# Kernel tuning notes

Measured on AMD Instinct MI355X. Metric: run time of the kernel, lower is better.

## Reference

```python
import jax, jax.numpy as jnp
import numpy as np

E, N, F = 50000, 25000, 32

def setup_inputs() -> dict:
    key = jax.random.key(0)
    ks = jax.random.split(key, 8)
    efeat = jax.random.normal(ks[0], (E, F), dtype=jnp.float32) * 0.2
    initial_efeats = jax.random.normal(ks[1], (E, F), dtype=jnp.float32) * 0.2
    # msg_fn / attn_fn: Linear(F, F*F)
    Wm = jax.random.normal(ks[2], (F * F, F), dtype=jnp.float32) * 0.05
    bm = jnp.zeros((F * F,), dtype=jnp.float32)
    Wa = jax.random.normal(ks[3], (F * F, F), dtype=jnp.float32) * 0.05
    ba = jnp.zeros((F * F,), dtype=jnp.float32)
    src = jax.random.randint(ks[4], (E,), 0, N, dtype=jnp.int32)
    dst = jax.random.randint(ks[5], (E,), 0, N, dtype=jnp.int32)
    return {"efeat": efeat, "initial_efeats": initial_efeats, "Wm": Wm, "bm": bm,
            "Wa": Wa, "ba": ba, "src": src, "dst": dst, "num_nodes": N}

def reference(efeat, initial_efeats, Wm, bm, Wa, ba, src, dst, num_nodes):
    e, f = efeat.shape
    # edge-conditioned transform matrices: [E, F, F]
    w_m = (efeat @ Wm.T + bm).reshape(e, f, f)
    w_a = (efeat @ Wa.T + ba).reshape(e, f, f)
    h = efeat[:, :, None]                 # [E, F, 1]
    ih = initial_efeats[:, :, None]       # [E, F, 1]
    e1 = w_m * h                          # [E, F, F]
    exp_e2 = jnp.exp(w_a * h)             # [E, F, F]
    initial_e1 = w_m * ih
    exp_initial_e2 = jnp.exp(w_a * ih)
    # scatter-sum exp weights to destination nodes, gather back at src
    sum_exp_node = jax.ops.segment_sum(exp_e2, dst, num_segments=num_nodes)  # [N, F, F]
    sum_exp = sum_exp_node[src] - exp_e2 + exp_initial_e2
    h1 = exp_e2 * e1
    initial_h1 = exp_initial_e2 * initial_e1
    m_node = jax.ops.segment_sum(h1, dst, num_segments=num_nodes)            # [N, F, F]
    h2 = (m_node[src] - h1 + initial_h1) / sum_exp
    return h2.sum(axis=1)                 # [E, F]
```

## Files before the change

kernel.cpp:

```cpp
#include <hip/hip_runtime.h>
#include <hip/hip_fp16.h>
#include <math.h>
#include <stdint.h>


#define FDIM   32
#define NNODES 25000

typedef __attribute__((ext_vector_type(8))) short bf16x8;
typedef __attribute__((ext_vector_type(4))) float f32x4;

__device__ __forceinline__ unsigned short f2bf(float f) {
    unsigned u = __float_as_uint(f);
    return (unsigned short)((u + 0x7FFFu + ((u >> 16) & 1u)) >> 16);
}
__device__ __forceinline__ float hlo(unsigned v) {
    return __half2float(__ushort_as_half((unsigned short)v));
}
__device__ __forceinline__ unsigned pk2(float m, float a) {
    unsigned um = (unsigned)__half_as_ushort(__float2half(m));
    unsigned ua = (unsigned)__half_as_ushort(__float2half(a));
    return (um >> 8) | (ua & 0xFF00u);
}

__global__ __launch_bounds__(256) void zero_f4(float4* __restrict__ p, int n4) {
    int i = blockIdx.x * blockDim.x + threadIdx.x;
    int stride = gridDim.x * blockDim.x;
    float4 z = make_float4(0.f, 0.f, 0.f, 0.f);
    for (; i < n4; i += stride) p[i] = z;
}

__global__ __launch_bounds__(256) void k_hist(
    const int* __restrict__ src, const int* __restrict__ dst,
    int* __restrict__ cnt_src, int* __restrict__ cnt_dst, int E) {
    int e = blockIdx.x * blockDim.x + threadIdx.x;
    if (e < E) {
        atomicAdd(&cnt_dst[dst[e]], 1);
        atomicAdd(&cnt_src[src[e]], 1);
    }
}

__global__ __launch_bounds__(256) void k_scan2(
    const int* __restrict__ cnt_dst, int* __restrict__ off_dst, int* __restrict__ cur_dst,
    const int* __restrict__ cnt_src, int* __restrict__ off_src, int* __restrict__ cur_src,
    int n) {
    const int* cnt = blockIdx.x ? cnt_src : cnt_dst;
    int* off = blockIdx.x ? off_src : off_dst;
    int* cur = blockIdx.x ? cur_src : cur_dst;
    __shared__ int wsum[4];
    __shared__ int carry_sh;
    const int tid = threadIdx.x, lane = tid & 63, w = tid >> 6;
    if (tid == 0) carry_sh = 0;
    __syncthreads();
    for (int base = 0; base < n; base += 1024) {
        int i0 = base + tid * 4;
        int v0 = (i0 + 0 < n) ? cnt[i0 + 0] : 0;
        int v1 = (i0 + 1 < n) ? cnt[i0 + 1] : 0;
        int v2 = (i0 + 2 < n) ? cnt[i0 + 2] : 0;
        int v3 = (i0 + 3 < n) ? cnt[i0 + 3] : 0;
        int s = v0 + v1 + v2 + v3;
        int inc = s;
        for (int d = 1; d < 64; d <<= 1) {
            int t = __shfl_up(inc, d, 64);
            if (lane >= d) inc += t;
        }
        if (lane == 63) wsum[w] = inc;
        __syncthreads();
        int wbase = 0;
        for (int k = 0; k < w; ++k) wbase += wsum[k];
        int carry = carry_sh;
        int excl = carry + wbase + inc - s;
        if (i0 + 0 < n) { off[i0 + 0] = excl; cur[i0 + 0] = excl; } excl += v0;
        if (i0 + 1 < n) { off[i0 + 1] = excl; cur[i0 + 1] = excl; } excl += v1;
        if (i0 + 2 < n) { off[i0 + 2] = excl; cur[i0 + 2] = excl; } excl += v2;
        if (i0 + 3 < n) { off[i0 + 3] = excl; cur[i0 + 3] = excl; }
        __syncthreads();
        if (tid == 255) carry_sh = carry + wbase + inc;
    }
    __syncthreads();
    if (tid == 0) off[n] = carry_sh;
}

__global__ __launch_bounds__(256) void k_scatter(
    const int* __restrict__ src, const int* __restrict__ dst,
    int* __restrict__ cur_src, int* __restrict__ cur_dst,
    int* __restrict__ eb_src, int* __restrict__ eb_dst, int E) {
    int e = blockIdx.x * blockDim.x + threadIdx.x;
    if (e < E) {
        int p = atomicAdd(&cur_dst[dst[e]], 1); eb_dst[p] = e;
        int q = atomicAdd(&cur_src[src[e]], 1); eb_src[q] = e;
    }
}

__global__ __launch_bounds__(256) void prep_w(
    const float* __restrict__ Wm, const float* __restrict__ Wa,
    short* __restrict__ wbuf) {
    int idx = blockIdx.x * blockDim.x + threadIdx.x;
    if (idx >= 2 * 64 * 64) return;
    int mat  = idx >> 12;
    int jt   = (idx >> 6) & 63;
    int lane = idx & 63;
    const float* W = mat ? Wa : Wm;
    const float* s = W + (size_t)(jt * 16 + (lane & 15)) * FDIM + (lane >> 4) * 8;
    bf16x8 v;
#pragma unroll
    for (int t = 0; t < 8; ++t) v[t] = (short)f2bf(s[t]);
    *(bf16x8*)(wbuf + (size_t)idx * 8) = v;
}

__global__ __launch_bounds__(256) void gemm(
    const float* __restrict__ efeat,
    const float* __restrict__ bm, const float* __restrict__ ba,
    const short* __restrict__ wbuf,
    unsigned short* __restrict__ buf, int E)
{
    const int lane = threadIdx.x & 63;
    const int wid  = threadIdx.x >> 6;
    const int et   = blockIdx.x * 4 + wid;
    if (et * 16 >= E) return;
    const int r16 = lane & 15;
    const int kq  = lane >> 4;

    const float* xa = efeat + (size_t)(et * 16 + r16) * FDIM + kq * 8;
    bf16x8 xfrag;
#pragma unroll
    for (int t = 0; t < 8; ++t) xfrag[t] = (short)f2bf(xa[t]);

    const int e = et * 16 + r16;
    unsigned* bout = (unsigned*)(buf + (size_t)e * 1024);

    for (int jt = 0; jt < 64; ++jt) {
        bf16x8 wfm = *(const bf16x8*)(wbuf + ((size_t)(jt)      * 64 + lane) * 8);
        bf16x8 wfa = *(const bf16x8*)(wbuf + ((size_t)(64 + jt) * 64 + lane) * 8);
        const int jb = jt * 16 + kq * 4;
        const float4 bm4 = *(const float4*)(bm + jb);
        const float4 ba4 = *(const float4*)(ba + jb);
        f32x4 accm = {bm4.x, bm4.y, bm4.z, bm4.w};
        f32x4 acca = {ba4.x, ba4.y, ba4.z, ba4.w};
        accm = __builtin_amdgcn_mfma_f32_16x16x32_bf16(wfm, xfrag, accm, 0, 0, 0);
        acca = __builtin_amdgcn_mfma_f32_16x16x32_bf16(wfa, xfrag, acca, 0, 0, 0);
        unsigned p0 = pk2(accm[0], acca[0]);
        unsigned p1 = pk2(accm[1], acca[1]);
        unsigned p2 = pk2(accm[2], acca[2]);
        unsigned p3 = pk2(accm[3], acca[3]);
        unsigned long long v = (unsigned long long)(p0 | (p1 << 16)) |
                               ((unsigned long long)(p2 | (p3 << 16)) << 32);
        *(unsigned long long*)(bout + (jb >> 1)) = v;
    }
}

__global__ __launch_bounds__(256) void consume(
    const float* __restrict__ efeat, const float* __restrict__ ifeat,
    const unsigned short* __restrict__ buf,
    const int* __restrict__ off_dst, const int* __restrict__ eb_dst,
    const int* __restrict__ off_src, const int* __restrict__ eb_src,
    float* __restrict__ out)
{
    const int tid = threadIdx.x;
    const int l   = tid & 63;
    const int wid = tid >> 6;
    const int n   = blockIdx.x * 4 + wid;
    if (n >= NNODES) return;

    const int a0 = off_dst[n], a1 = off_dst[n + 1];
    const int b0 = off_src[n], b1 = off_src[n + 1];
    const int din = a1 - a0, dout = b1 - b0;
    if (dout == 0) return;

    int eid = (l < 32) ? eb_dst[a0 + l] : eb_src[b0 + (l - 32)];
    const int i = l >> 1;

    float S[16], M[16];
#pragma unroll
    for (int t = 0; t < 16; ++t) { S[t] = 0.f; M[t] = 0.f; }

    for (int t = 0; t < din; ++t) {
        int e = (t < 32) ? __shfl(eid, t, 64) : eb_dst[a0 + t];
        e = __builtin_amdgcn_readfirstlane(e);
        const uint4* bp = (const uint4*)(buf + ((size_t)e << 10) + l * 16);
        uint4 d0 = bp[0], d1 = bp[1];
        float xi = efeat[((size_t)e << 5) + i];
        unsigned u[8] = {d0.x, d0.y, d0.z, d0.w, d1.x, d1.y, d1.z, d1.w};
#pragma unroll
        for (int w = 0; w < 8; ++w) {
            unsigned uu = u[w];
            float am0 = hlo(uu << 8),  aa0 = hlo(uu);
            float am1 = hlo(uu >> 8),  aa1 = hlo(uu >> 16);
            float ea = __expf(aa0 * xi);
            float eb = __expf(aa1 * xi);
            S[2 * w]     += ea;  M[2 * w]     = fmaf(ea, am0 * xi, M[2 * w]);
            S[2 * w + 1] += eb;  M[2 * w + 1] = fmaf(eb, am1 * xi, M[2 * w + 1]);
        }
    }

    for (int t = 0; t < dout; ++t) {
        int e = (t < 32) ? __shfl(eid, 32 + t, 64) : eb_src[b0 + t];
        e = __builtin_amdgcn_readfirstlane(e);
        const uint4* bp = (const uint4*)(buf + ((size_t)e << 10) + l * 16);
        uint4 d0 = bp[0], d1 = bp[1];
        float xi  = efeat[((size_t)e << 5) + i];
        float x0i = ifeat[((size_t)e << 5) + i];
        unsigned u[8] = {d0.x, d0.y, d0.z, d0.w, d1.x, d1.y, d1.z, d1.w};
        float acc[16];
#pragma unroll
        for (int w = 0; w < 8; ++w) {
            unsigned uu = u[w];
            float am0 = hlo(uu << 8),  aa0 = hlo(uu);
            float am1 = hlo(uu >> 8),  aa1 = hlo(uu >> 16);
#define PROC(T2, AM, AA)                                                \
            {                                                           \
                float amx  = (AM) * xi;                                 \
                float e2   = __expf((AA) * xi);                         \
                float h1   = e2 * amx;                                  \
                float ei2  = __expf((AA) * x0i);                        \
                float ih1  = ei2 * ((AM) * x0i);                        \
                float den  = (S[T2] - e2) + ei2;                        \
                float num  = (M[T2] - h1) + ih1;                        \
                float h2   = num * __builtin_amdgcn_rcpf(den);          \
                acc[T2] = isfinite(h2) ? h2 : 0.f;                      \
            }
            PROC(2 * w,     am0, aa0);
            PROC(2 * w + 1, am1, aa1);
#undef PROC
        }
#pragma unroll
        for (int t2 = 0; t2 < 16; ++t2) {
            acc[t2] += __shfl_xor(acc[t2], 2, 64);
            acc[t2] += __shfl_xor(acc[t2], 4, 64);
            acc[t2] += __shfl_xor(acc[t2], 8, 64);
            acc[t2] += __shfl_xor(acc[t2], 16, 64);
            acc[t2] += __shfl_xor(acc[t2], 32, 64);
        }
        if (l < 2) {
            float4* o = (float4*)(out + ((size_t)e << 5) + l * 16);
            o[0] = make_float4(acc[0],  acc[1],  acc[2],  acc[3]);
            o[1] = make_float4(acc[4],  acc[5],  acc[6],  acc[7]);
            o[2] = make_float4(acc[8],  acc[9],  acc[10], acc[11]);
            o[3] = make_float4(acc[12], acc[13], acc[14], acc[15]);
        }
    }
}

extern "C" void kernel_launch(void* const* d_in, const int* in_sizes, int n_in,
                              void* d_out, int out_size, void* d_ws, size_t ws_size,
                              hipStream_t stream) {
    const float* efeat = (const float*)d_in[0];
    const float* ifeat = (const float*)d_in[1];
    const float* Wm    = (const float*)d_in[2];
    const float* bm    = (const float*)d_in[3];
    const float* Wa    = (const float*)d_in[4];
    const float* ba    = (const float*)d_in[5];
    const int*   src   = (const int*)d_in[6];
    const int*   dst   = (const int*)d_in[7];
    const int E = in_sizes[6];
    const int N = NNODES;
    float* out = (float*)d_out;

    int* cnt_dst = (int*)d_ws;
    int* cnt_src = cnt_dst + N;
    int* off_dst = cnt_src + N;
    int* off_src = off_dst + (N + 1);
    int* cur_dst = off_src + (N + 1);
    int* cur_src = cur_dst + N;
    int* eb_dst  = cur_src + N;
    int* eb_src  = eb_dst + E;
    short* wbuf  = (short*)(((uintptr_t)(eb_src + E) + 255) & ~(uintptr_t)255);
    unsigned short* buf =
        (unsigned short*)(((uintptr_t)(wbuf + 2 * 64 * 64 * 8) + 255) & ~(uintptr_t)255);

    zero_f4<<<64, 256, 0, stream>>>((float4*)cnt_dst, (2 * N) / 4);
    k_hist<<<(E + 255) / 256, 256, 0, stream>>>(src, dst, cnt_src, cnt_dst, E);
    k_scan2<<<2, 256, 0, stream>>>(cnt_dst, off_dst, cur_dst,
                                   cnt_src, off_src, cur_src, N);
    k_scatter<<<(E + 255) / 256, 256, 0, stream>>>(src, dst, cur_src, cur_dst,
                                                   eb_src, eb_dst, E);
    prep_w<<<32, 256, 0, stream>>>(Wm, Wa, wbuf);

    const int etiles = (E + 15) / 16;
    gemm<<<(etiles + 3) / 4, 256, 0, stream>>>(efeat, bm, ba, wbuf, buf, E);
    consume<<<(NNODES + 3) / 4, 256, 0, stream>>>(efeat, ifeat, buf,
                                                  off_dst, eb_dst,
                                                  off_src, eb_src, out);
}
```

Before: 260.2 us.

## Transpose intermediate buffer layout so consume reduces over rows in-lane

The gemm output buffer is re-laid out so each lane in consume owns one output column j and walks 16 rows i, interleaving pairs of rows in each 32-bit word. This replaces the per-edge 16-value, 5-step cross-lane shuffle reduction with an in-register sum plus one xor shuffle, and loads efeat/ifeat rows as vector float4 reads. Consume now issues strided 4-byte loads from buf instead of contiguous 32-byte loads, which may reduce coalescing. The scan kernel also processes 16 elements per thread per iteration instead of 4.

```diff
diff --git a/kernel.cpp b/kernel.cpp
--- a/kernel.cpp
+++ b/kernel.cpp
@@ -52,13 +52,15 @@
     const int tid = threadIdx.x, lane = tid & 63, w = tid >> 6;
     if (tid == 0) carry_sh = 0;
     __syncthreads();
-    for (int base = 0; base < n; base += 1024) {
-        int i0 = base + tid * 4;
-        int v0 = (i0 + 0 < n) ? cnt[i0 + 0] : 0;
-        int v1 = (i0 + 1 < n) ? cnt[i0 + 1] : 0;
-        int v2 = (i0 + 2 < n) ? cnt[i0 + 2] : 0;
-        int v3 = (i0 + 3 < n) ? cnt[i0 + 3] : 0;
-        int s = v0 + v1 + v2 + v3;
+    for (int base = 0; base < n; base += 4096) {
+        int i0 = base + tid * 16;
+        int v[16];
+        int s = 0;
+#pragma unroll
+        for (int k = 0; k < 16; ++k) {
+            v[k] = (i0 + k < n) ? cnt[i0 + k] : 0;
+            s += v[k];
+        }
         int inc = s;
         for (int d = 1; d < 64; d <<= 1) {
             int t = __shfl_up(inc, d, 64);
@@ -70,10 +72,11 @@
         for (int k = 0; k < w; ++k) wbase += wsum[k];
         int carry = carry_sh;
         int excl = carry + wbase + inc - s;
-        if (i0 + 0 < n) { off[i0 + 0] = excl; cur[i0 + 0] = excl; } excl += v0;
-        if (i0 + 1 < n) { off[i0 + 1] = excl; cur[i0 + 1] = excl; } excl += v1;
-        if (i0 + 2 < n) { off[i0 + 2] = excl; cur[i0 + 2] = excl; } excl += v2;
-        if (i0 + 3 < n) { off[i0 + 3] = excl; cur[i0 + 3] = excl; }
+#pragma unroll
+        for (int k = 0; k < 16; ++k) {
+            if (i0 + k < n) { off[i0 + k] = excl; cur[i0 + k] = excl; }
+            excl += v[k];
+        }
         __syncthreads();
         if (tid == 255) carry_sh = carry + wbase + inc;
     }
@@ -112,7 +115,7 @@
     const float* __restrict__ efeat,
     const float* __restrict__ bm, const float* __restrict__ ba,
     const short* __restrict__ wbuf,
-    unsigned short* __restrict__ buf, int E)
+    unsigned* __restrict__ buf, int E)
 {
     const int lane = threadIdx.x & 63;
     const int wid  = threadIdx.x >> 6;
@@ -127,31 +130,42 @@
     for (int t = 0; t < 8; ++t) xfrag[t] = (short)f2bf(xa[t]);
 
     const int e = et * 16 + r16;
-    unsigned* bout = (unsigned*)(buf + (size_t)e * 1024);
-
-    for (int jt = 0; jt < 64; ++jt) {
-        bf16x8 wfm = *(const bf16x8*)(wbuf + ((size_t)(jt)      * 64 + lane) * 8);
-        bf16x8 wfa = *(const bf16x8*)(wbuf + ((size_t)(64 + jt) * 64 + lane) * 8);
-        const int jb = jt * 16 + kq * 4;
-        const float4 bm4 = *(const float4*)(bm + jb);
-        const float4 ba4 = *(const float4*)(ba + jb);
-        f32x4 accm = {bm4.x, bm4.y, bm4.z, bm4.w};
-        f32x4 acca = {ba4.x, ba4.y, ba4.z, ba4.w};
-        accm = __builtin_amdgcn_mfma_f32_16x16x32_bf16(wfm, xfrag, accm, 0, 0, 0);
-        acca = __builtin_amdgcn_mfma_f32_16x16x32_bf16(wfa, xfrag, acca, 0, 0, 0);
-        unsigned p0 = pk2(accm[0], acca[0]);
-        unsigned p1 = pk2(accm[1], acca[1]);
-        unsigned p2 = pk2(accm[2], acca[2]);
-        unsigned p3 = pk2(accm[3], acca[3]);
-        unsigned long long v = (unsigned long long)(p0 | (p1 << 16)) |
-                               ((unsigned long long)(p2 | (p3 << 16)) << 32);
-        *(unsigned long long*)(bout + (jb >> 1)) = v;
+    unsigned* bout = buf + ((size_t)e << 9);
+
+    for (int m = 0; m < 16; ++m) {
+        unsigned P[4][4];
+#pragma unroll
+        for (int p = 0; p < 4; ++p) {
+            const int jt = m * 4 + p;
+            bf16x8 wfm = *(const bf16x8*)(wbuf + ((size_t)(jt)      * 64 + lane) * 8);
+            bf16x8 wfa = *(const bf16x8*)(wbuf + ((size_t)(64 + jt) * 64 + lane) * 8);
+            const int jb = jt * 16 + kq * 4;
+            const float4 bm4 = *(const float4*)(bm + jb);
+            const float4 ba4 = *(const float4*)(ba + jb);
+            f32x4 accm = {bm4.x, bm4.y, bm4.z, bm4.w};
+            f32x4 acca = {ba4.x, ba4.y, ba4.z, ba4.w};
+            accm = __builtin_amdgcn_mfma_f32_16x16x32_bf16(wfm, xfrag, accm, 0, 0, 0);
+            acca = __builtin_amdgcn_mfma_f32_16x16x32_bf16(wfa, xfrag, acca, 0, 0, 0);
+#pragma unroll
+            for (int r = 0; r < 4; ++r) P[p][r] = pk2(accm[r], acca[r]);
+        }
+        uint4 sa, sb;
+        sa.x = P[0][0] | (P[2][0] << 16);
+        sa.y = P[0][1] | (P[2][1] << 16);
+        sa.z = P[0][2] | (P[2][2] << 16);
+        sa.w = P[0][3] | (P[2][3] << 16);
+        sb.x = P[1][0] | (P[3][0] << 16);
+        sb.y = P[1][1] | (P[3][1] << 16);
+        sb.z = P[1][2] | (P[3][2] << 16);
+        sb.w = P[1][3] | (P[3][3] << 16);
+        *(uint4*)(bout + m * 32 + kq * 4)      = sa;
+        *(uint4*)(bout + m * 32 + 16 + kq * 4) = sb;
     }
 }
 
 __global__ __launch_bounds__(256) void consume(
     const float* __restrict__ efeat, const float* __restrict__ ifeat,
-    const unsigned short* __restrict__ buf,
+    const unsigned* __restrict__ buf,
     const int* __restrict__ off_dst, const int* __restrict__ eb_dst,
     const int* __restrict__ off_src, const int* __restrict__ eb_src,
     float* __restrict__ out)
@@ -168,7 +182,9 @@
     if (dout == 0) return;
 
     int eid = (l < 32) ? eb_dst[a0 + l] : eb_src[b0 + (l - 32)];
-    const int i = l >> 1;
+    const int half = l & 1;
+    const int j2   = l >> 1;
+    const int mb   = half * 8;
 
     float S[16], M[16];
 #pragma unroll
@@ -177,67 +193,82 @@
     for (int t = 0; t < din; ++t) {
         int e = (t < 32) ? __shfl(eid, t, 64) : eb_dst[a0 + t];
         e = __builtin_amdgcn_readfirstlane(e);
-        const uint4* bp = (const uint4*)(buf + ((size_t)e << 10) + l * 16);
-        uint4 d0 = bp[0], d1 = bp[1];
-        float xi = efeat[((size_t)e << 5) + i];
-        unsigned u[8] = {d0.x, d0.y, d0.z, d0.w, d1.x, d1.y, d1.z, d1.w};
-#pragma unroll
-        for (int w = 0; w < 8; ++w) {
-            unsigned uu = u[w];
-            float am0 = hlo(uu << 8),  aa0 = hlo(uu);
-            float am1 = hlo(uu >> 8),  aa1 = hlo(uu >> 16);
-            float ea = __expf(aa0 * xi);
-            float eb = __expf(aa1 * xi);
-            S[2 * w]     += ea;  M[2 * w]     = fmaf(ea, am0 * xi, M[2 * w]);
-            S[2 * w + 1] += eb;  M[2 * w + 1] = fmaf(eb, am1 * xi, M[2 * w + 1]);
+        const unsigned* bp = buf + ((size_t)e << 9) + j2;
+        const float* xr = efeat + ((size_t)e << 5) + half * 16;
+        float xf[16];
+        {
+            float4 q0 = *(const float4*)(xr + 0);
+            float4 q1 = *(const float4*)(xr + 4);
+            float4 q2 = *(const float4*)(xr + 8);
+            float4 q3 = *(const float4*)(xr + 12);
+            xf[0]=q0.x; xf[1]=q0.y; xf[2]=q0.z; xf[3]=q0.w;
+            xf[4]=q1.x; xf[5]=q1.y; xf[6]=q1.z; xf[7]=q1.w;
+            xf[8]=q2.x; xf[9]=q2.y; xf[10]=q2.z; xf[11]=q2.w;
+            xf[12]=q3.x; xf[13]=q3.y; xf[14]=q3.z; xf[15]=q3.w;
+        }
+#pragma unroll
+        for (int s = 0; s < 8; ++s) {
+            unsigned d = bp[(mb + s) * 32];
+            float am0 = hlo(d << 8),  aa0 = hlo(d);
+            float am1 = hlo(d >> 8),  aa1 = hlo(d >> 16);
+            float xi0 = xf[2 * s], xi1 = xf[2 * s + 1];
+            float ea = __expf(aa0 * xi0);
+            float eb = __expf(aa1 * xi1);
+            S[2 * s]     += ea;  M[2 * s]     = fmaf(ea, am0 * xi0, M[2 * s]);
+            S[2 * s + 1] += eb;  M[2 * s + 1] = fmaf(eb, am1 * xi1, M[2 * s + 1]);
         }
     }
 
     for (int t = 0; t < dout; ++t) {
         int e = (t < 32) ? __shfl(eid, 32 + t, 64) : eb_src[b0 + t];
         e = __builtin_amdgcn_readfirstlane(e);
-        const uint4* bp = (const uint4*)(buf + ((size_t)e << 10) + l * 16);
-        uint4 d0 = bp[0], d1 = bp[1];
-        float xi  = efeat[((size_t)e << 5) + i];
-        float x0i = ifeat[((size_t)e << 5) + i];
-        unsigned u[8] = {d0.x, d0.y, d0.z, d0.w, d1.x, d1.y, d1.z, d1.w};
-        float acc[16];
-#pragma unroll
-        for (int w = 0; w < 8; ++w) {
-            unsigned uu = u[w];
-            float am0 = hlo(uu << 8),  aa0 = hlo(uu);
-            float am1 = hlo(uu >> 8),  aa1 = hlo(uu >> 16);
-#define PROC(T2, AM, AA)                                                \
+        const unsigned* bp = buf + ((size_t)e << 9) + j2;
+        const float* xr  = efeat + ((size_t)e << 5) + half * 16;
+        const float* x0r = ifeat + ((size_t)e << 5) + half * 16;
+        float xf[16], x0f[16];
+        {
+            float4 q0 = *(const float4*)(xr + 0);
+            float4 q1 = *(const float4*)(xr + 4);
+            float4 q2 = *(const float4*)(xr + 8);
+            float4 q3 = *(const float4*)(xr + 12);
+            xf[0]=q0.x; xf[1]=q0.y; xf[2]=q0.z; xf[3]=q0.w;
+            xf[4]=q1.x; xf[5]=q1.y; xf[6]=q1.z; xf[7]=q1.w;
+            xf[8]=q2.x; xf[9]=q2.y; xf[10]=q2.z; xf[11]=q2.w;
+            xf[12]=q3.x; xf[13]=q3.y; xf[14]=q3.z; xf[15]=q3.w;
+            float4 p0 = *(const float4*)(x0r + 0);
+            float4 p1 = *(const float4*)(x0r + 4);
+            float4 p2 = *(const float4*)(x0r + 8);
+            float4 p3 = *(const float4*)(x0r + 12);
+            x0f[0]=p0.x; x0f[1]=p0.y; x0f[2]=p0.z; x0f[3]=p0.w;
+            x0f[4]=p1.x; x0f[5]=p1.y; x0f[6]=p1.z; x0f[7]=p1.w;
+            x0f[8]=p2.x; x0f[9]=p2.y; x0f[10]=p2.z; x0f[11]=p2.w;
+            x0f[12]=p3.x; x0f[13]=p3.y; x0f[14]=p3.z; x0f[15]=p3.w;
+        }
+        float osum = 0.f;
+#pragma unroll
+        for (int s = 0; s < 8; ++s) {
+            unsigned d = bp[(mb + s) * 32];
+            float am0 = hlo(d << 8),  aa0 = hlo(d);
+            float am1 = hlo(d >> 8),  aa1 = hlo(d >> 16);
+#define PROC(T, AM, AA)                                                 \
             {                                                           \
-                float amx  = (AM) * xi;                                 \
+                float xi   = xf[T];                                     \
+                float x0i  = x0f[T];                                    \
                 float e2   = __expf((AA) * xi);                         \
-                float h1   = e2 * amx;                                  \
+                float h1   = e2 * ((AM) * xi);                          \
                 float ei2  = __expf((AA) * x0i);                        \
                 float ih1  = ei2 * ((AM) * x0i);                        \
-                float den  = (S[T2] - e2) + ei2;                        \
-                float num  = (M[T2] - h1) + ih1;                        \
+                float den  = (S[T] - e2) + ei2;                         \
+                float num  = (M[T] - h1) + ih1;                         \
                 float h2   = num * __builtin_amdgcn_rcpf(den);          \
-                acc[T2] = isfinite(h2) ? h2 : 0.f;                      \
+                osum += isfinite(h2) ? h2 : 0.f;                        \
             }
-            PROC(2 * w,     am0, aa0);
-            PROC(2 * w + 1, am1, aa1);
+            PROC(2 * s,     am0, aa0);
+            PROC(2 * s + 1, am1, aa1);
 #undef PROC
         }
-#pragma unroll
-        for (int t2 = 0; t2 < 16; ++t2) {
-            acc[t2] += __shfl_xor(acc[t2], 2, 64);
-            acc[t2] += __shfl_xor(acc[t2], 4, 64);
-            acc[t2] += __shfl_xor(acc[t2], 8, 64);
-            acc[t2] += __shfl_xor(acc[t2], 16, 64);
-            acc[t2] += __shfl_xor(acc[t2], 32, 64);
-        }
-        if (l < 2) {
-            float4* o = (float4*)(out + ((size_t)e << 5) + l * 16);
-            o[0] = make_float4(acc[0],  acc[1],  acc[2],  acc[3]);
-            o[1] = make_float4(acc[4],  acc[5],  acc[6],  acc[7]);
-            o[2] = make_float4(acc[8],  acc[9],  acc[10], acc[11]);
-            o[3] = make_float4(acc[12], acc[13], acc[14], acc[15]);
-        }
+        osum += __shfl_xor(osum, 1, 64);
+        if (half == 0) out[((size_t)e << 5) + j2] = osum;
     }
 }
 
@@ -265,8 +296,8 @@
     int* eb_dst  = cur_src + N;
     int* eb_src  = eb_dst + E;
     short* wbuf  = (short*)(((uintptr_t)(eb_src + E) + 255) & ~(uintptr_t)255);
-    unsigned short* buf =
-        (unsigned short*)(((uintptr_t)(wbuf + 2 * 64 * 64 * 8) + 255) & ~(uintptr_t)255);
+    unsigned* buf =
+        (unsigned*)(((uintptr_t)(wbuf + 2 * 64 * 64 * 8) + 255) & ~(uintptr_t)255);
 
     zero_f4<<<64, 256, 0, stream>>>((float4*)cnt_dst, (2 * N) / 4);
     k_hist<<<(E + 255) / 256, 256, 0, stream>>>(src, dst, cnt_src, cnt_dst, E);
```

After: 244.2 us. 6.2% less time.
